# Performance work log

Hardware: AMD Instinct MI355X
Metric: run time of the kernel (lower is better)

The kernel has to match this reference:

```python
import math
import jax, jax.numpy as jnp
import numpy as np

B, L, D, H = 8, 512, 768, 12
DK = D // H  # 64


def setup_inputs() -> dict:
    key = jax.random.key(0)
    ks = jax.random.split(key, 8)
    x = jax.random.normal(ks[0], (B, L, D), dtype=jnp.float32)
    mask = jnp.zeros((B, L), dtype=jnp.float32)            # 0 = valid, -10000 = pad (torch convention here)
    roots_label = jax.random.randint(ks[1], (B, L), 0, 2, dtype=jnp.int32)
    root_mask = jnp.ones((B, L), dtype=jnp.int32)          # only checked for not-None in the original
    W_SCALE = 0.02  # keep exp(scores) well-conditioned, as trained weights would
    Wq = jax.random.normal(ks[2], (D, D), dtype=jnp.float32) * W_SCALE
    bq = jnp.zeros((D,), dtype=jnp.float32)
    Wk = jax.random.normal(ks[3], (D, D), dtype=jnp.float32) * W_SCALE
    bk = jnp.zeros((D,), dtype=jnp.float32)
    Wr = jax.random.normal(ks[4], (D, 1), dtype=jnp.float32) * W_SCALE
    br = jnp.zeros((1,), dtype=jnp.float32)
    return {"x": x, "mask": mask, "roots_label": roots_label, "root_mask": root_mask,
            "Wq": Wq, "bq": bq, "Wk": Wk, "bk": bk, "Wr": Wr, "br": br}


def _matrix_tree_multi(scores, root):
    # scores: [B,H,L,L], root: [B,L,1]  (multi-head branch of _getMatrixTree_multi)
    A = jnp.exp(scores)                                   # [B,H,L,L]
    R = jnp.broadcast_to(jnp.exp(root)[..., 0][:, None, :], A.shape[:3])  # [B,H,L]
    col_sum = jnp.sum(A, axis=2)                          # [B,H,L]  (torch.sum(A, 2))
    eye = jnp.eye(A.shape[-1], dtype=A.dtype)
    # LL = diag(col_sum) - A + diag(R)
    LL = (col_sum + R)[..., :, None] * eye - A * (1.0 - eye) - A * eye + A * eye  # keep exact: diag(col_sum+R) - A
    LL = (col_sum + R)[..., :, None] * eye - A
    LL_inv = jnp.linalg.inv(LL)                           # [B,H,L,L]
    LL_inv_diag = jnp.diagonal(LL_inv, axis1=-2, axis2=-1)  # [B,H,L]
    d0 = R * LL_inv_diag                                  # root marginals [B,H,L]
    tmp1 = A * LL_inv_diag[..., None, :]                  # = transpose(A^T * diag[...,:,None])
    tmp2 = A * jnp.swapaxes(LL_inv, -2, -1)
    d = tmp1 - tmp2                                       # edge marginals [B,H,L,L]
    return d, d0


def reference(x, mask, roots_label, root_mask, Wq, bq, Wk, bk, Wr, br):
    key = x @ Wk + bk                                     # [B,L,D]
    query = (x @ Wq + bq) / math.sqrt(D)
    root = x @ Wr + br                                    # [B,L,1]
    q = query.reshape(B, L, H, DK).transpose(0, 2, 1, 3)  # [B,H,L,DK]
    k = key.reshape(B, L, H, DK).transpose(0, 2, 1, 3)
    scores = jnp.einsum('bhqd,bhkd->bhqk', q, k)          # [B,H,L,L]
    m = mask / -10000.0                                   # 1 at padded positions
    root = jnp.clip(root - m[:, :, None] * 50.0, -40.0, None)
    sm = jnp.broadcast_to(m[:, None, :, None], (B, H, L, L))  # scores_mask
    scores = jnp.clip(scores - sm * 50.0 - jnp.swapaxes(sm, -2, -1) * 50.0, -40.0, None)
    d, d0 = _matrix_tree_multi(scores, root)
    # root BCE loss summed over heads, masked-mean with labels
    labels = roots_label.reshape(-1).astype(jnp.float32)  # [B*L]
    p = jnp.clip(d0.astype(jnp.float32), 1e-5, 1.0 - 1e-5)
    p_h = jnp.moveaxis(p, 1, 0).reshape(H, -1)            # [H, B*L]
    bce = -(labels * jnp.log(p_h) + (1.0 - labels) * jnp.log(1.0 - p_h))
    loss_root = (bce.sum(axis=0) * labels).mean()
    attn = jnp.swapaxes(d, -2, -1)
    sm_sym = (sm + jnp.swapaxes(sm, -2, -1)).astype(bool)
    attn = jnp.where(sm_sym, 0.0, attn)
    context = jnp.einsum('bhqk,bkd->bhqd', attn, x)       # [B,H,L,D]
    return context, d, d0, loss_root
```

## Files before the change

### kernel.cpp

```cpp
#include <hip/hip_runtime.h>
#include <hip/hip_bf16.h>
#include <math.h>


#define INV_SQRT_D 0.03608439182435161f

typedef short bf16x8 __attribute__((ext_vector_type(8)));
typedef float f32x4 __attribute__((ext_vector_type(4)));
typedef unsigned int u32x4 __attribute__((ext_vector_type(4)));

__device__ __forceinline__ void mm_micro(const float* At, const float* Bt,
                                         float acc[8][8], int tx, int ty)
{
#pragma unroll
  for (int t = 0; t < 16; ++t) {
    const float4 a0 = *(const float4*)(At + t*132 + ty*8);
    const float4 a1 = *(const float4*)(At + t*132 + ty*8 + 4);
    const float4 b0 = *(const float4*)(Bt + t*132 + tx*8);
    const float4 b1 = *(const float4*)(Bt + t*132 + tx*8 + 4);
    const float a[8] = {a0.x,a0.y,a0.z,a0.w,a1.x,a1.y,a1.z,a1.w};
    const float b[8] = {b0.x,b0.y,b0.z,b0.w,b1.x,b1.y,b1.z,b1.w};
#pragma unroll
    for (int i = 0; i < 8; ++i)
#pragma unroll
      for (int j = 0; j < 8; ++j)
        acc[i][j] = fmaf(a[i], b[j], acc[i][j]);
  }
}

__global__ __launch_bounds__(256) void proj_kernel(
    const float* __restrict__ x,
    const float* __restrict__ Wq, const float* __restrict__ bq,
    const float* __restrict__ Wk, const float* __restrict__ bk,
    float* __restrict__ Q, float* __restrict__ Kc)
{
  const float* W; const float* bias; float* out; float scale;
  if (blockIdx.z == 0) { W = Wq; bias = bq; out = Q;  scale = INV_SQRT_D; }
  else                 { W = Wk; bias = bk; out = Kc; scale = 1.0f; }

  __shared__ __align__(16) float At[16*132];
  __shared__ __align__(16) float Bt[16*132];

  const int tx = threadIdx.x, ty = threadIdx.y;
  const int tid = ty*16 + tx;
  const int row0 = blockIdx.y * 128, col0 = blockIdx.x * 128;
  const int lt = tid & 15, lr = tid >> 4;
  const int bc = tid & 127, btr = tid >> 7;

  float acc[8][8] = {};

  for (int kk = 0; kk < 768; kk += 16) {
#pragma unroll
    for (int u = 0; u < 8; ++u) {
      const int r = lr + 16*u;
      At[lt*132 + r] = x[(size_t)(row0 + r)*768 + kk + lt];
    }
#pragma unroll
    for (int u = 0; u < 8; ++u) {
      const int t = btr + 2*u;
      Bt[t*132 + bc] = W[(size_t)(kk + t)*768 + col0 + bc];
    }
    __syncthreads();
    mm_micro(At, Bt, acc, tx, ty);
    __syncthreads();
  }

#pragma unroll
  for (int i = 0; i < 8; ++i) {
    const int r = row0 + ty*8 + i;
#pragma unroll
    for (int j = 0; j < 8; j += 4) {
      const int c = col0 + tx*8 + j;
      float4 v;
      v.x = (acc[i][j+0] + bias[c+0]) * scale;
      v.y = (acc[i][j+1] + bias[c+1]) * scale;
      v.z = (acc[i][j+2] + bias[c+2]) * scale;
      v.w = (acc[i][j+3] + bias[c+3]) * scale;
      *(float4*)(out + (size_t)r*768 + c) = v;
    }
  }
}

__global__ __launch_bounds__(256) void root_kernel(
    const float* __restrict__ x, const float* __restrict__ Wr,
    const float* __restrict__ br, const float* __restrict__ mask,
    float* __restrict__ Rv, float* __restrict__ mv)
{
  const int n = blockIdx.x*4 + (threadIdx.x >> 6);
  const int lane = threadIdx.x & 63;
  float s = 0.0f;
  for (int c = lane; c < 768; c += 64) s += x[(size_t)n*768 + c] * Wr[c];
#pragma unroll
  for (int off = 32; off > 0; off >>= 1) s += __shfl_down(s, off, 64);
  if (lane == 0) {
    const float root = s + br[0];
    const float m = mask[n] * (-1e-4f);
    Rv[n] = expf(fmaxf(root - m*50.0f, -40.0f));
    mv[n] = m;
  }
}

__global__ __launch_bounds__(256) void scores_kernel(
    const float* __restrict__ Qs, const float* __restrict__ Ks,
    const float* __restrict__ mv, float* __restrict__ A)
{
  const int bh = blockIdx.z, b = bh / 12, h = bh % 12;
  const int i0 = blockIdx.y * 128, j0 = blockIdx.x * 128;
  __shared__ __align__(16) float At[16*132];
  __shared__ __align__(16) float Bt[16*132];
  const int tx = threadIdx.x, ty = threadIdx.y;
  const int tid = ty*16 + tx;
  const int lt = tid & 15, lr = tid >> 4;
  const size_t qbase = (size_t)(b*512 + i0)*768 + h*64;
  const size_t kbase = (size_t)(b*512 + j0)*768 + h*64;

  float acc[8][8] = {};

  for (int kk = 0; kk < 64; kk += 16) {
#pragma unroll
    for (int u = 0; u < 8; ++u) {
      const int r = lr + 16*u;
      At[lt*132 + r] = Qs[qbase + (size_t)r*768 + kk + lt];
      Bt[lt*132 + r] = Ks[kbase + (size_t)r*768 + kk + lt];
    }
    __syncthreads();
    mm_micro(At, Bt, acc, tx, ty);
    __syncthreads();
  }

  float mi[8], mj[8];
#pragma unroll
  for (int i = 0; i < 8; ++i) mi[i] = mv[b*512 + i0 + ty*8 + i];
#pragma unroll
  for (int j = 0; j < 8; ++j) mj[j] = mv[b*512 + j0 + tx*8 + j];

#pragma unroll
  for (int i = 0; i < 8; ++i) {
    const size_t rowb = (size_t)(bh*512 + i0 + ty*8 + i)*512;
#pragma unroll
    for (int j = 0; j < 8; j += 4) {
      float4 v;
      v.x = expf(fmaxf(acc[i][j+0] - (mi[i]+mj[j+0])*50.0f, -40.0f));
      v.y = expf(fmaxf(acc[i][j+1] - (mi[i]+mj[j+1])*50.0f, -40.0f));
      v.z = expf(fmaxf(acc[i][j+2] - (mi[i]+mj[j+2])*50.0f, -40.0f));
      v.w = expf(fmaxf(acc[i][j+3] - (mi[i]+mj[j+3])*50.0f, -40.0f));
      *(float4*)(A + rowb + j0 + tx*8 + j) = v;
    }
  }
}

__global__ void colsum_kernel(const float* __restrict__ A, float* __restrict__ colsum)
{
  const int bh = blockIdx.y;
  const int j = blockIdx.x*256 + threadIdx.x;
  const float* Ab = A + (size_t)bh*262144;
  float s = 0.0f;
  for (int i = 0; i < 512; ++i) s += Ab[(size_t)i*512 + j];
  colsum[bh*512 + j] = s;
}

__global__ void buildM_kernel(const float* __restrict__ A, const float* __restrict__ colsum,
                              const float* __restrict__ Rv, float* __restrict__ M)
{
  const size_t g = ((size_t)blockIdx.x*256 + threadIdx.x)*4;
  const int bh = (int)(g >> 18);
  const int i = (int)((g >> 9) & 511);
  const int j = (int)(g & 511);
  const float4 a = *(const float4*)(A + g);
  float4 v; v.x = -a.x; v.y = -a.y; v.z = -a.z; v.w = -a.w;
  if (i >= j && i < j+4) {
    const float dadd = colsum[bh*512 + i] + Rv[(bh/12)*512 + i];
    ((float*)&v)[i - j] += dadd;
  }
  *(float4*)(M + g) = v;
}

__global__ __launch_bounds__(256) void gj_inv_kernel(
    const float* __restrict__ M, float* __restrict__ Mp,
    float* __restrict__ Inv, int k0)
{
  const float* const Mg  = M   + (size_t)blockIdx.x * 262144;
  float* const Mpg       = Mp  + (size_t)blockIdx.x * 32768;
  float* const Ig        = Inv + (size_t)blockIdx.x * 4096;
  const int tid = threadIdx.x;

  if (tid >= 64) {
    const int t = tid - 64;
    for (int p = 0; p < 43; ++p) {
      const int idx = p*192 + t;
      if (idx < 8192) {
        const int r = idx >> 7, c = (idx & 127) * 4;
        *(float4*)(Mpg + (size_t)r*512 + c) =
            *(const float4*)(Mg + (size_t)(k0 + r)*512 + c);
      }
    }
    return;
  }

  const int lane = tid;
  float w[64];
  {
    const float* src = Mg + (size_t)(k0 + lane)*512 + k0;
#pragma unroll
    for (int q = 0; q < 16; ++q) {
      const float4 t4 = *(const float4*)(src + q*4);
      w[q*4+0]=t4.x; w[q*4+1]=t4.y; w[q*4+2]=t4.z; w[q*4+3]=t4.w;
    }
  }

  float fcur = w[0];
#pragma unroll 1
  for (int kk = 0; kk < 64; ++kk) {
    const float pv = __shfl(fcur, kk);
    const float p  = 1.0f / pv;
    const float fp = fcur * p;
    const bool isp = (lane == kk);
    const float alpha = isp ? p : -fp;
    const float beta  = isp ? 0.0f : 1.0f;
    float fnext = fcur;
#pragma unroll
    for (int j = 0; j < 64; ++j) {
      const float rj = __shfl(w[j], kk);
      float nv = fmaf(alpha, rj, beta * w[j]);
      const float val = (j == kk) ? alpha : nv;
      if (j == kk + 1) fnext = val;
      w[j] = val;
    }
    fcur = fnext;
  }

  {
    float* dst = Ig + lane*64;
#pragma unroll
    for (int q = 0; q < 16; ++q)
      *(float4*)(dst + q*4) = make_float4(w[q*4+0], w[q*4+1], w[q*4+2], w[q*4+3]);
  }
}

__global__ __launch_bounds__(256) void gj_w_kernel(
    float* __restrict__ M, const float* __restrict__ Inv, int k0)
{
  const int bh = blockIdx.y;
  const int row0 = blockIdx.x * 128;
  float* const Mg = M + (size_t)bh*262144;
  const float* const Ig = Inv + (size_t)bh*4096;

  __shared__ __align__(16) float Ct[16*132];
  __shared__ __align__(16) float It[16*68];

  const int tx = threadIdx.x, ty = threadIdx.y;
  const int tid = ty*16 + tx;
  const int lt = tid & 15, lr = tid >> 4;

  float acc[8][4] = {};

  for (int kc = 0; kc < 64; kc += 16) {
#pragma unroll
    for (int u = 0; u < 8; ++u) {
      const int r = lr + 16*u;
      Ct[lt*132 + r] = Mg[(size_t)(row0 + r)*512 + k0 + kc + lt];
    }
    {
      const int j = tid & 63, t0 = tid >> 6;
#pragma unroll
      for (int u = 0; u < 4; ++u) {
        const int t = t0*4 + u;
        It[t*68 + j] = Ig[(kc + t)*64 + j];
      }
    }
    __syncthreads();
#pragma unroll
    for (int t = 0; t < 16; ++t) {
      const float4 a0 = *(const float4*)(Ct + t*132 + ty*8);
      const float4 a1 = *(const float4*)(Ct + t*132 + ty*8 + 4);
      const float4 b  = *(const float4*)(It + t*68 + tx*4);
      const float a[8] = {a0.x,a0.y,a0.z,a0.w,a1.x,a1.y,a1.z,a1.w};
      const float bb[4] = {b.x,b.y,b.z,b.w};
#pragma unroll
      for (int i = 0; i < 8; ++i)
#pragma unroll
        for (int j = 0; j < 4; ++j)
          acc[i][j] = fmaf(a[i], bb[j], acc[i][j]);
    }
    __syncthreads();
  }

#pragma unroll
  for (int i = 0; i < 8; ++i) {
    const int irow = row0 + ty*8 + i;
    float4 v;
    if (irow >= k0 && irow < k0 + 64) {
      v = *(const float4*)(Ig + (irow - k0)*64 + tx*4);
    } else {
      v = make_float4(-acc[i][0], -acc[i][1], -acc[i][2], -acc[i][3]);
    }
    *(float4*)(Mg + (size_t)irow*512 + k0 + tx*4) = v;
  }
}

__global__ __launch_bounds__(256) void gj_update_kernel(
    float* __restrict__ M, const float* __restrict__ Mp, int k0)
{
  const int bh = blockIdx.z;
  const int row0 = blockIdx.y * 128, col0 = blockIdx.x * 128;
  float* const Mg = M + (size_t)bh*262144;
  const float* const Mpg = Mp + (size_t)bh*32768;

  __shared__ __align__(16) float At[16*132];
  __shared__ __align__(16) float Bt[16*132];
  const int tx = threadIdx.x, ty = threadIdx.y;
  const int tid = ty*16 + tx;
  const int lt = tid & 15, lr = tid >> 4;
  const int bc = tid & 127, btr = tid >> 7;

  float acc[8][8] = {};

  for (int kc = 0; kc < 64; kc += 16) {
#pragma unroll
    for (int u = 0; u < 8; ++u) {
      const int r = lr + 16*u;
      At[lt*132 + r] = Mg[(size_t)(row0 + r)*512 + k0 + kc + lt];
    }
#pragma unroll
    for (int u = 0; u < 8; ++u) {
      const int t = btr + 2*u;
      Bt[t*132 + bc] = Mpg[(size_t)(kc + t)*512 + col0 + bc];
    }
    __syncthreads();
    mm_micro(At, Bt, acc, tx, ty);
    __syncthreads();
  }

#pragma unroll
  for (int ii = 0; ii < 8; ++ii) {
    const int irow = row0 + ty*8 + ii;
    const bool inP = (irow >= k0) && (irow < k0 + 64);
#pragma unroll
    for (int jj = 0; jj < 8; jj += 4) {
      const int jcol = col0 + tx*8 + jj;
      if (jcol >= k0 && jcol < k0 + 64) continue;
      float* cell = Mg + (size_t)irow*512 + jcol;
      float4 v = make_float4(acc[ii][jj+0], acc[ii][jj+1], acc[ii][jj+2], acc[ii][jj+3]);
      if (!inP) {
        const float4 o = *(const float4*)cell;
        v.x += o.x; v.y += o.y; v.z += o.z; v.w += o.w;
      }
      *(float4*)cell = v;
    }
  }
}

__global__ void diag_d0_kernel(const float* __restrict__ Minv, const float* __restrict__ Rv,
                               float* __restrict__ diagv, float* __restrict__ d0)
{
  const int bh = blockIdx.x, l = threadIdx.x;
  const float dg = Minv[(size_t)bh*262144 + (size_t)l*513];
  diagv[bh*512 + l] = dg;
  d0[bh*512 + l] = Rv[(bh/12)*512 + l] * dg;
}

__global__ __launch_bounds__(1024) void loss_kernel(const float* __restrict__ d0,
                                                    const int* __restrict__ labels,
                                                    float* __restrict__ loss)
{
  float acc = 0.0f;
  for (int n = threadIdx.x; n < 4096; n += 1024) {
    if (labels[n] != 0) {
      const int b = n >> 9, l = n & 511;
      float s = 0.0f;
#pragma unroll
      for (int h = 0; h < 12; ++h) {
        float p = d0[(size_t)(b*12 + h)*512 + l];
        p = fminf(fmaxf(p, 1e-5f), 1.0f - 1e-5f);
        s -= logf(p);
      }
      acc += s;
    }
  }
  __shared__ float red[16];
#pragma unroll
  for (int off = 32; off > 0; off >>= 1) acc += __shfl_down(acc, off, 64);
  const int wv = threadIdx.x >> 6, ln = threadIdx.x & 63;
  if (ln == 0) red[wv] = acc;
  __syncthreads();
  if (threadIdx.x == 0) {
    float t = 0.0f;
    for (int w2 = 0; w2 < 16; ++w2) t += red[w2];
    loss[0] = t * (1.0f/4096.0f);
  }
}

__global__ __launch_bounds__(256) void finalize_d_kernel(
    float* __restrict__ dmat, const float* __restrict__ Minv, const float* __restrict__ diagv)
{
  const int bh = blockIdx.z;
  const int i0 = blockIdx.y*64, j0 = blockIdx.x*64;
  __shared__ float t[64][65];
  const int tx = threadIdx.x, ty = threadIdx.y;
  const size_t mbase = (size_t)bh*262144;
  for (int jj = ty; jj < 64; jj += 4)
    t[jj][tx] = Minv[mbase + (size_t)(j0+jj)*512 + i0 + tx];
  __syncthreads();
  const float dg_j = diagv[bh*512 + j0 + tx];
  for (int ii = ty; ii < 64; ii += 4) {
    const size_t idx = mbase + (size_t)(i0+ii)*512 + j0 + tx;
    dmat[idx] = dmat[idx] * (dg_j - t[tx][ii]);
  }
}

__device__ __forceinline__ unsigned int pack_bf16x2(float v)
{
  const unsigned int u = __float_as_uint(v);
  const unsigned int hi = (u + 0x7FFFu + ((u >> 16) & 1u)) >> 16;
  const float hf = __uint_as_float(hi << 16);
  const unsigned int lo = __float_as_uint(v - hf) >> 16;
  return hi | (lo << 16);
}

__global__ __launch_bounds__(256) void context_mfma_kernel(
    const float* __restrict__ dmat, const float* __restrict__ x,
    const float* __restrict__ mv, float* __restrict__ ctx)
{
  const int bh = blockIdx.z, b = bh / 12;
  const int q0 = blockIdx.y << 7;
  const int c0 = blockIdx.x << 7;

  __shared__ unsigned int As[32*133];
  __shared__ unsigned int Bs[32*133];

  const int tid = threadIdx.x;
  const int w = tid >> 6, l = tid & 63;
  const int wq = w >> 1, wc = w & 1;
  const int l15 = l & 15, g = l >> 4;
  const int q4 = tid & 31, kr0 = tid >> 5;

  const size_t dbase = (size_t)bh*262144;
  const size_t xbase = (size_t)b*393216;

  float mq[4];
  {
    const float4 t4 = *(const float4*)(mv + b*512 + q0 + q4*4);
    mq[0]=t4.x; mq[1]=t4.y; mq[2]=t4.z; mq[3]=t4.w;
  }

  f32x4 acc[4][4] = {};

  for (int kk = 0; kk < 512; kk += 32) {
    __syncthreads();
#pragma unroll
    for (int p = 0; p < 4; ++p) {
      const int kr = kr0 + 8*p;
      const int krow = kk + kr;
      const float mk = mv[b*512 + krow];
      const float4 av = *(const float4*)(dmat + dbase + (size_t)krow*512 + q0 + q4*4);
      const float4 bv = *(const float4*)(x + xbase + (size_t)krow*768 + c0 + q4*4);
      unsigned int* aw = As + kr*133 + q4*4;
      unsigned int* bw = Bs + kr*133 + q4*4;
      aw[0] = pack_bf16x2(((mk + mq[0]) != 0.0f) ? 0.0f : av.x);
      aw[1] = pack_bf16x2(((mk + mq[1]) != 0.0f) ? 0.0f : av.y);
      aw[2] = pack_bf16x2(((mk + mq[2]) != 0.0f) ? 0.0f : av.z);
      aw[3] = pack_bf16x2(((mk + mq[3]) != 0.0f) ? 0.0f : av.w);
      bw[0] = pack_bf16x2(bv.x);
      bw[1] = pack_bf16x2(bv.y);
      bw[2] = pack_bf16x2(bv.z);
      bw[3] = pack_bf16x2(bv.w);
    }
    __syncthreads();

    u32x4 ah[4], al[4], bhv[4], blv[4];
#pragma unroll
    for (int mi = 0; mi < 4; ++mi) {
      const unsigned int* base = As + g*8*133 + (wq*64 + mi*16 + l15);
      unsigned int u[8];
#pragma unroll
      for (int e = 0; e < 8; ++e) u[e] = base[e*133];
#pragma unroll
      for (int d2 = 0; d2 < 4; ++d2) {
        ah[mi][d2] = __builtin_amdgcn_perm(u[2*d2+1], u[2*d2], 0x05040100u);
        al[mi][d2] = __builtin_amdgcn_perm(u[2*d2+1], u[2*d2], 0x07060302u);
      }
    }
#pragma unroll
    for (int ni = 0; ni < 4; ++ni) {
      const unsigned int* base = Bs + g*8*133 + (wc*64 + ni*16 + l15);
      unsigned int u[8];
#pragma unroll
      for (int e = 0; e < 8; ++e) u[e] = base[e*133];
#pragma unroll
      for (int d2 = 0; d2 < 4; ++d2) {
        bhv[ni][d2] = __builtin_amdgcn_perm(u[2*d2+1], u[2*d2], 0x05040100u);
        blv[ni][d2] = __builtin_amdgcn_perm(u[2*d2+1], u[2*d2], 0x07060302u);
      }
    }

#pragma unroll
    for (int mi = 0; mi < 4; ++mi) {
      const bf16x8 Ah = __builtin_bit_cast(bf16x8, ah[mi]);
      const bf16x8 Al = __builtin_bit_cast(bf16x8, al[mi]);
#pragma unroll
      for (int ni = 0; ni < 4; ++ni) {
        const bf16x8 Bh = __builtin_bit_cast(bf16x8, bhv[ni]);
        const bf16x8 Bl = __builtin_bit_cast(bf16x8, blv[ni]);
        acc[mi][ni] = __builtin_amdgcn_mfma_f32_16x16x32_bf16(Ah, Bh, acc[mi][ni], 0, 0, 0);
        acc[mi][ni] = __builtin_amdgcn_mfma_f32_16x16x32_bf16(Ah, Bl, acc[mi][ni], 0, 0, 0);
        acc[mi][ni] = __builtin_amdgcn_mfma_f32_16x16x32_bf16(Al, Bh, acc[mi][ni], 0, 0, 0);
      }
    }
  }

#pragma unroll
  for (int mi = 0; mi < 4; ++mi) {
    const int row = q0 + wq*64 + mi*16 + g*4;
#pragma unroll
    for (int ni = 0; ni < 4; ++ni) {
      const int col = c0 + wc*64 + ni*16 + l15;
#pragma unroll
      for (int r = 0; r < 4; ++r)
        ctx[((size_t)bh*512 + row + r)*768 + col] = acc[mi][ni][r];
    }
  }
}

extern "C" void kernel_launch(void* const* d_in, const int* in_sizes, int n_in,
                              void* d_out, int out_size, void* d_ws, size_t ws_size,
                              hipStream_t stream)
{
  (void)in_sizes; (void)n_in; (void)out_size; (void)ws_size;

  const float* x    = (const float*)d_in[0];
  const float* mask = (const float*)d_in[1];
  const int*   roots= (const int*)d_in[2];
  const float* Wq   = (const float*)d_in[4];
  const float* bq   = (const float*)d_in[5];
  const float* Wk   = (const float*)d_in[6];
  const float* bk   = (const float*)d_in[7];
  const float* Wr   = (const float*)d_in[8];
  const float* br   = (const float*)d_in[9];

  float* out        = (float*)d_out;
  float* ctx_region = out;
  float* d_region   = out + 37748736;
  float* d0_region  = out + 62914560;
  float* loss_ptr   = out + 62963712;

  float* Qs = ctx_region;
  float* Ks = ctx_region + 3145728;
  float* Mv = ctx_region + 6291456;
  float* Mp = ctx_region + 31457280;
  float* Invs = ctx_region + 34603008;

  float* ws     = (float*)d_ws;
  float* Rv     = ws;
  float* mv     = ws + 4096;
  float* colsum = ws + 8192;
  float* diagv  = ws + 57344;

  proj_kernel   <<<dim3(6,32,2),  dim3(16,16), 0, stream>>>(x, Wq, bq, Wk, bk, Qs, Ks);
  root_kernel   <<<dim3(1024),    dim3(256),   0, stream>>>(x, Wr, br, mask, Rv, mv);
  scores_kernel <<<dim3(4,4,96),  dim3(16,16), 0, stream>>>(Qs, Ks, mv, d_region);
  colsum_kernel <<<dim3(2,96),    dim3(256),   0, stream>>>(d_region, colsum);
  buildM_kernel <<<dim3(24576),   dim3(256),   0, stream>>>(d_region, colsum, Rv, Mv);

  for (int step = 0; step < 8; ++step) {
    const int k0 = step * 64;
    gj_inv_kernel   <<<dim3(96),     dim3(256),   0, stream>>>(Mv, Mp, Invs, k0);
    gj_w_kernel     <<<dim3(4,96),   dim3(16,16), 0, stream>>>(Mv, Invs, k0);
    gj_update_kernel<<<dim3(4,4,96), dim3(16,16), 0, stream>>>(Mv, Mp, k0);
  }

  diag_d0_kernel<<<dim3(96),      dim3(512),   0, stream>>>(Mv, Rv, diagv, d0_region);
  loss_kernel   <<<dim3(1),       dim3(1024),  0, stream>>>(d0_region, roots, loss_ptr);
  finalize_d_kernel<<<dim3(8,8,96), dim3(64,4), 0, stream>>>(d_region, Mv, diagv);
  context_mfma_kernel<<<dim3(6,4,96), dim3(256), 0, stream>>>(d_region, x, mv, ctx_region);
}
```

Before: 1.902 ms.

## Pre-pack x into split bf16 hi/lo once and restructure context GEMM

Adds a kernel that converts x once into packed hi/lo bf16 pairs, so the context kernel stops re-splitting x for every (b,h) tile. A new packed context kernel handles heads 8..95 by reading the pre-split x. Heads 0..7 stay on the old kernel because the packed buffers alias the ctx output region those heads write. The Gauss-Jordan inner loop also hoists all row shuffles ahead of the update loop and removes a multiply, at the cost of more register pressure.

Measured after the change: 1.909 ms. About the same (+0.3%).

```diff
diff --git a/kernel.cpp b/kernel.cpp
--- a/kernel.cpp
+++ b/kernel.cpp
@@ -149,6 +149,35 @@
   }
 }
 
+__global__ __launch_bounds__(256) void pack_x_kernel(
+    const float* __restrict__ x, unsigned int* __restrict__ xh,
+    unsigned int* __restrict__ xl)
+{
+  const int gid = blockIdx.x*256 + threadIdx.x;
+  const int k2g = gid / 192;
+  const int cc  = (gid - k2g*192) * 4;
+  const unsigned int* xb = (const unsigned int*)x;
+  const size_t s0 = (size_t)(2*k2g)*768 + cc;
+  const uint4 r0 = *(const uint4*)(xb + s0);
+  const uint4 r1 = *(const uint4*)(xb + s0 + 768);
+  unsigned int hw[4], lw[4];
+#pragma unroll
+  for (int i = 0; i < 4; ++i) {
+    const unsigned int u0 = ((const unsigned int*)&r0)[i];
+    const unsigned int u1 = ((const unsigned int*)&r1)[i];
+    const unsigned int h0 = (u0 + 0x7FFFu + ((u0 >> 16) & 1u)) >> 16;
+    const unsigned int h1 = (u1 + 0x7FFFu + ((u1 >> 16) & 1u)) >> 16;
+    hw[i] = h0 | (h1 << 16);
+    const float rs0 = __uint_as_float(u0) - __uint_as_float(h0 << 16);
+    const float rs1 = __uint_as_float(u1) - __uint_as_float(h1 << 16);
+    lw[i] = __builtin_amdgcn_perm(__float_as_uint(rs1), __float_as_uint(rs0),
+                                  0x07060302u);
+  }
+  const size_t o = (size_t)k2g*768 + cc;
+  *(uint4*)(xh + o) = make_uint4(hw[0], hw[1], hw[2], hw[3]);
+  *(uint4*)(xl + o) = make_uint4(lw[0], lw[1], lw[2], lw[3]);
+}
+
 __global__ void colsum_kernel(const float* __restrict__ A, float* __restrict__ colsum)
 {
   const int bh = blockIdx.y;
@@ -211,20 +240,21 @@
   float fcur = w[0];
 #pragma unroll 1
   for (int kk = 0; kk < 64; ++kk) {
+    float rj[64];
+#pragma unroll
+    for (int j = 0; j < 64; ++j) rj[j] = __shfl(w[j], kk);
     const float pv = __shfl(fcur, kk);
     const float p  = 1.0f / pv;
-    const float fp = fcur * p;
     const bool isp = (lane == kk);
-    const float alpha = isp ? p : -fp;
-    const float beta  = isp ? 0.0f : 1.0f;
+    const float alpha = isp ? p : -fcur * p;
     float fnext = fcur;
 #pragma unroll
     for (int j = 0; j < 64; ++j) {
-      const float rj = __shfl(w[j], kk);
-      float nv = fmaf(alpha, rj, beta * w[j]);
-      const float val = (j == kk) ? alpha : nv;
+      const float base = isp ? 0.0f : w[j];
+      float val = fmaf(alpha, rj[j], base);
+      if (j == kk) val = alpha;
+      w[j] = val;
       if (j == kk + 1) fnext = val;
-      w[j] = val;
     }
     fcur = fnext;
   }
@@ -405,6 +435,116 @@
   for (int ii = ty; ii < 64; ii += 4) {
     const size_t idx = mbase + (size_t)(i0+ii)*512 + j0 + tx;
     dmat[idx] = dmat[idx] * (dg_j - t[tx][ii]);
+  }
+}
+
+__global__ __launch_bounds__(256) void context_packed_kernel(
+    const float* __restrict__ dmat, const unsigned int* __restrict__ xh,
+    const unsigned int* __restrict__ xl, const float* __restrict__ mv,
+    float* __restrict__ ctx)
+{
+  const int bh = blockIdx.z + 8, b = bh / 12;
+  const int q0 = blockIdx.y << 7;
+  const int c0 = blockIdx.x << 7;
+
+  __shared__ __align__(16) unsigned int AhL[16*132];
+  __shared__ __align__(16) unsigned int AlL[16*132];
+  __shared__ __align__(16) unsigned int BhL[16*132];
+  __shared__ __align__(16) unsigned int BlL[16*132];
+
+  const int tid = threadIdx.x;
+  const int w = tid >> 6, l = tid & 63;
+  const int wq = w >> 1, wc = w & 1;
+  const int l15 = l & 15, g = l >> 4;
+  const int q4 = tid & 31, pp = tid >> 5;
+
+  const size_t dbase = (size_t)bh*262144;
+  const int xrow0 = b*256;
+
+  float mq[4];
+  {
+    const float4 t4 = *(const float4*)(mv + b*512 + q0 + q4*4);
+    mq[0]=t4.x; mq[1]=t4.y; mq[2]=t4.z; mq[3]=t4.w;
+  }
+
+  f32x4 acc[4][4] = {};
+
+  for (int kk = 0; kk < 512; kk += 32) {
+    __syncthreads();
+#pragma unroll
+    for (int s = 0; s < 2; ++s) {
+      const int k2 = pp + 8*s;
+      const int krow = kk + 2*k2;
+      const float mk0 = mv[b*512 + krow];
+      const float mk1 = mv[b*512 + krow + 1];
+      const uint4 r0 = *(const uint4*)(dmat + dbase + (size_t)krow*512 + q0 + q4*4);
+      const uint4 r1 = *(const uint4*)(dmat + dbase + (size_t)(krow+1)*512 + q0 + q4*4);
+      unsigned int hw[4], lw[4];
+#pragma unroll
+      for (int i = 0; i < 4; ++i) {
+        unsigned int v0 = ((const unsigned int*)&r0)[i];
+        unsigned int v1 = ((const unsigned int*)&r1)[i];
+        v0 = ((mk0 + mq[i]) != 0.0f) ? 0u : v0;
+        v1 = ((mk1 + mq[i]) != 0.0f) ? 0u : v1;
+        hw[i] = __builtin_amdgcn_perm(v1, v0, 0x07060302u);
+        const float f0 = __uint_as_float(v0) - __uint_as_float(v0 & 0xffff0000u);
+        const float f1 = __uint_as_float(v1) - __uint_as_float(v1 & 0xffff0000u);
+        lw[i] = __builtin_amdgcn_perm(__float_as_uint(f1), __float_as_uint(f0),
+                                      0x07060302u);
+      }
+      *(uint4*)(AhL + k2*132 + q4*4) = make_uint4(hw[0], hw[1], hw[2], hw[3]);
+      *(uint4*)(AlL + k2*132 + q4*4) = make_uint4(lw[0], lw[1], lw[2], lw[3]);
+      const size_t xi = (size_t)(xrow0 + (kk >> 1) + k2)*768 + c0 + q4*4;
+      *(uint4*)(BhL + k2*132 + q4*4) = *(const uint4*)(xh + xi);
+      *(uint4*)(BlL + k2*132 + q4*4) = *(const uint4*)(xl + xi);
+    }
+    __syncthreads();
+
+    u32x4 ah[4], al[4], bhv[4], blv[4];
+#pragma unroll
+    for (int mi = 0; mi < 4; ++mi) {
+      const int col = wq*64 + mi*16 + l15;
+#pragma unroll
+      for (int d2 = 0; d2 < 4; ++d2) {
+        ah[mi][d2] = AhL[(4*g + d2)*132 + col];
+        al[mi][d2] = AlL[(4*g + d2)*132 + col];
+      }
+    }
+#pragma unroll
+    for (int ni = 0; ni < 4; ++ni) {
+      const int col = wc*64 + ni*16 + l15;
+#pragma unroll
+      for (int d2 = 0; d2 < 4; ++d2) {
+        bhv[ni][d2] = BhL[(4*g + d2)*132 + col];
+        blv[ni][d2] = BlL[(4*g + d2)*132 + col];
+      }
+    }
+
+#pragma unroll
+    for (int mi = 0; mi < 4; ++mi) {
+      const bf16x8 Ah = __builtin_bit_cast(bf16x8, ah[mi]);
+      const bf16x8 Al = __builtin_bit_cast(bf16x8, al[mi]);
+#pragma unroll
+      for (int ni = 0; ni < 4; ++ni) {
+        const bf16x8 Bh = __builtin_bit_cast(bf16x8, bhv[ni]);
+        const bf16x8 Bl = __builtin_bit_cast(bf16x8, blv[ni]);
+        acc[mi][ni] = __builtin_amdgcn_mfma_f32_16x16x32_bf16(Ah, Bh, acc[mi][ni], 0, 0, 0);
+        acc[mi][ni] = __builtin_amdgcn_mfma_f32_16x16x32_bf16(Ah, Bl, acc[mi][ni], 0, 0, 0);
+        acc[mi][ni] = __builtin_amdgcn_mfma_f32_16x16x32_bf16(Al, Bh, acc[mi][ni], 0, 0, 0);
+      }
+    }
+  }
+
+#pragma unroll
+  for (int mi = 0; mi < 4; ++mi) {
+    const int row = q0 + wq*64 + mi*16 + g*4;
+#pragma unroll
+    for (int ni = 0; ni < 4; ++ni) {
+      const int col = c0 + wc*64 + ni*16 + l15;
+#pragma unroll
+      for (int r = 0; r < 4; ++r)
+        ctx[((size_t)bh*512 + row + r)*768 + col] = acc[mi][ni][r];
+    }
   }
 }
 
@@ -549,6 +689,9 @@
   float* Mp = ctx_region + 31457280;
   float* Invs = ctx_region + 34603008;
 
+  unsigned int* xh = (unsigned int*)ctx_region;
+  unsigned int* xl = (unsigned int*)ctx_region + 1572864;
+
   float* ws     = (float*)d_ws;
   float* Rv     = ws;
   float* mv     = ws + 4096;
@@ -558,6 +701,7 @@
   proj_kernel   <<<dim3(6,32,2),  dim3(16,16), 0, stream>>>(x, Wq, bq, Wk, bk, Qs, Ks);
   root_kernel   <<<dim3(1024),    dim3(256),   0, stream>>>(x, Wr, br, mask, Rv, mv);
   scores_kernel <<<dim3(4,4,96),  dim3(16,16), 0, stream>>>(Qs, Ks, mv, d_region);
+  pack_x_kernel <<<dim3(1536),    dim3(256),   0, stream>>>(x, xh, xl);
   colsum_kernel <<<dim3(2,96),    dim3(256),   0, stream>>>(d_region, colsum);
   buildM_kernel <<<dim3(24576),   dim3(256),   0, stream>>>(d_region, colsum, Rv, Mv);
 
@@ -571,5 +715,6 @@
   diag_d0_kernel<<<dim3(96),      dim3(512),   0, stream>>>(Mv, Rv, diagv, d0_region);
   loss_kernel   <<<dim3(1),       dim3(1024),  0, stream>>>(d0_region, roots, loss_ptr);
   finalize_d_kernel<<<dim3(8,8,96), dim3(64,4), 0, stream>>>(d_region, Mv, diagv);
-  context_mfma_kernel<<<dim3(6,4,96), dim3(256), 0, stream>>>(d_region, x, mv, ctx_region);
-}
+  context_packed_kernel<<<dim3(6,4,88), dim3(256), 0, stream>>>(d_region, xh, xl, mv, ctx_region);
+  context_mfma_kernel  <<<dim3(6,4,8),  dim3(256), 0, stream>>>(d_region, x, mv, ctx_region);
+}
```
